# Kernel tuning notes

Hardware: AMD Instinct MI355X
Metric: run time of the kernel (lower is better)

Reference implementation:

```python
import jax, jax.numpy as jnp
import numpy as np
import math

ROPE_THETA = 10000.0


def apply_rope(x, positions):
    # x: [B, H, S, d_k], positions: [S]
    d_k = x.shape[-1]
    inv_freq = 1.0 / (ROPE_THETA ** (jnp.arange(0, d_k, 2, dtype=jnp.float32) / d_k))  # [d_k/2]
    angles = positions.astype(jnp.float32)[:, None] * inv_freq[None, :]  # [S, d_k/2]
    cos = jnp.cos(angles)
    sin = jnp.sin(angles)
    x1 = x[..., 0::2]
    x2 = x[..., 1::2]
    r1 = x1 * cos - x2 * sin
    r2 = x1 * sin + x2 * cos
    out = jnp.stack([r1, r2], axis=-1)  # interleave pairs back
    return out.reshape(x.shape)


def setup_inputs() -> dict:
    key = jax.random.key(0)
    k1, k2, k3 = jax.random.split(key, 3)
    B, S, D = 4, 2048, 1024
    x = jax.random.normal(k1, (B, S, D), dtype=jnp.float32)
    token_positions = jnp.arange(S, dtype=jnp.int32)
    w_qkv = jax.random.normal(k2, (3 * D, D), dtype=jnp.float32) * (1.0 / math.sqrt(D))
    w_o = jax.random.normal(k3, (D, D), dtype=jnp.float32) * (1.0 / math.sqrt(D))
    return {"x": x, "token_positions": token_positions, "w_qkv": w_qkv, "w_o": w_o}


def reference(x, token_positions, w_qkv, w_o):
    B, S, D = x.shape
    H = 16
    d_k = D // H
    qkv = jnp.einsum('bsd,ed->bse', x, w_qkv)  # [B, S, 3D]
    # rearrange '... s (stack h dk) -> stack ... h s dk'
    qkv = qkv.reshape(B, S, 3, H, d_k)
    q = jnp.transpose(qkv[:, :, 0], (0, 2, 1, 3))  # [B, H, S, dk]
    k = jnp.transpose(qkv[:, :, 1], (0, 2, 1, 3))
    v = jnp.transpose(qkv[:, :, 2], (0, 2, 1, 3))
    q = apply_rope(q, token_positions)
    k = apply_rope(k, token_positions)
    scores = jnp.einsum('bhqd,bhkd->bhqk', q, k) / math.sqrt(d_k)
    causal = jnp.tril(jnp.ones((S, S), dtype=bool))
    scores = jnp.where(causal[None, None], scores, -jnp.inf)
    attn = jax.nn.softmax(scores, axis=-1)
    out = jnp.einsum('bhqk,bhkd->bhqd', attn, v)  # [B, H, S, dk]
    out = jnp.transpose(out, (0, 2, 1, 3)).reshape(B, S, D)
    return jnp.einsum('bsd,ed->bse', out, w_o)
```

## Files before the change

kernel.cpp:

```cpp
#include <hip/hip_runtime.h>
#include <hip/hip_bf16.h>
#include <math.h>

typedef __bf16 bf16_t;
typedef __attribute__((ext_vector_type(8))) __bf16 bf16x8;
typedef __attribute__((ext_vector_type(4))) __bf16 bf16x4;
typedef __attribute__((ext_vector_type(4))) float f32x4;

#define MFMA_16x16x32(A_, B_, C_) __builtin_amdgcn_mfma_f32_16x16x32_bf16((A_), (B_), (C_), 0, 0, 0)

#define Bsz 4
#define Ssz 2048
#define Dsz 1024
#define Hh 16
#define DKd 64
#define Mrows (Bsz * Ssz)
#define N1 (3 * Dsz)
#define KD Dsz

static __device__ __forceinline__ float fast_exp2(float x) {
  float r;
  asm("v_exp_f32 %0, %1" : "=v"(r) : "v"(x));
  return r;
}

__global__ void prep_kernel(const float* __restrict__ x, const float* __restrict__ wqkv,
                            const float* __restrict__ wo, const int* __restrict__ pos,
                            bf16_t* __restrict__ xb, bf16_t* __restrict__ wqkvb,
                            bf16_t* __restrict__ wob, float2* __restrict__ tab) {
  constexpr int N4X = Mrows * KD / 4;
  constexpr int N4W = N1 * KD / 4;
  constexpr int N4O = Dsz * KD / 4;
  constexpr int NRT = Ssz * 32;
  const int i = blockIdx.x * blockDim.x + threadIdx.x;
  if (i < N4X) {
    float4 v = reinterpret_cast<const float4*>(x)[i];
    bf16x4 o = {(bf16_t)v.x, (bf16_t)v.y, (bf16_t)v.z, (bf16_t)v.w};
    reinterpret_cast<bf16x4*>(xb)[i] = o;
  } else if (i < N4X + N4W) {
    const int j = i - N4X;
    float4 v = reinterpret_cast<const float4*>(wqkv)[j];
    bf16x4 o = {(bf16_t)v.x, (bf16_t)v.y, (bf16_t)v.z, (bf16_t)v.w};
    reinterpret_cast<bf16x4*>(wqkvb)[j] = o;
  } else if (i < N4X + N4W + N4O) {
    const int j = i - N4X - N4W;
    float4 v = reinterpret_cast<const float4*>(wo)[j];
    bf16x4 o = {(bf16_t)v.x, (bf16_t)v.y, (bf16_t)v.z, (bf16_t)v.w};
    reinterpret_cast<bf16x4*>(wob)[j] = o;
  } else if (i < N4X + N4W + N4O + NRT) {
    const int j = i - N4X - N4W - N4O;
    const int s = j >> 5, f = j & 31;
    float inv_freq = powf(10000.0f, -(float)(2 * f) / 64.0f);
    float a = (float)pos[s] * inv_freq;
    tab[j] = make_float2(cosf(a), sinf(a));
  }
}

__global__ __launch_bounds__(512, 1) void gemm256_qkv_kernel(
    const bf16_t* __restrict__ A, const bf16_t* __restrict__ Bt,
    bf16_t* __restrict__ qb, bf16_t* __restrict__ kb, bf16_t* __restrict__ vtb,
    const float2* __restrict__ tab) {
  constexpr int NT = KD / 64;
  __shared__ __align__(16) bf16_t As[2][256 * 64];
  __shared__ __align__(16) bf16_t Bs[2][192 * 64];
  const int t = threadIdx.x;
  const int w = t >> 6, l = t & 63;
  const int lr = l & 15, lk = l >> 4;
  const int rs = lr >> 1;
  const int wm = w >> 2, wn = w & 3;
  const int m0 = blockIdx.y * 256, n0 = blockIdx.x * 192;

  const int gcol = ((t & 7) ^ ((t >> 4) & 7)) * 8;
  const bf16_t* gA = A + (size_t)(m0 + (t >> 3)) * KD + gcol;
  const bf16_t* gB = Bt + (size_t)(n0 + (t >> 3)) * KD + gcol;

  f32x4 acc[8][3] = {};
  bf16x8 bfv[3][2];

#define LDA_(I_, SB_, KT_)                                                        \
  __builtin_amdgcn_global_load_lds(gA + (size_t)(I_) * 64 * KD + (KT_),           \
                                   &As[SB_][((I_) * 64 + w * 8) * 64], 16, 0, 0)
#define LDB_(I_, SB_, KT_)                                                        \
  __builtin_amdgcn_global_load_lds(gB + (size_t)(I_) * 64 * KD + (KT_),           \
                                   &Bs[SB_][((I_) * 64 + w * 8) * 64], 16, 0, 0)

#define PH(BUF_, P_, STG0_, STG1_, VMW_)                                          \
  do {                                                                            \
    if ((P_) == 0) {                                                              \
      _Pragma("unroll") for (int n_ = 0; n_ < 3; ++n_) {                          \
        const int R_ = wn * 48 + n_ * 16 + lr;                                    \
        bfv[n_][0] = *reinterpret_cast<const bf16x8*>(                            \
            &Bs[BUF_][R_ * 64 + ((lk ^ rs) * 8)]);                                \
        bfv[n_][1] = *reinterpret_cast<const bf16x8*>(                            \
            &Bs[BUF_][R_ * 64 + (((4 + lk) ^ rs) * 8)]);                          \
      }                                                                           \
    }                                                                             \
    bf16x8 af0_[2], af1_[2];                                                      \
    {                                                                             \
      const int Ra_ = wm * 128 + (P_) * 32 + lr;                                  \
      const int Rb_ = Ra_ + 16;                                                   \
      af0_[0] = *reinterpret_cast<const bf16x8*>(&As[BUF_][Ra_ * 64 + ((lk ^ rs) * 8)]);       \
      af0_[1] = *reinterpret_cast<const bf16x8*>(&As[BUF_][Ra_ * 64 + (((4 + lk) ^ rs) * 8)]); \
      af1_[0] = *reinterpret_cast<const bf16x8*>(&As[BUF_][Rb_ * 64 + ((lk ^ rs) * 8)]);       \
      af1_[1] = *reinterpret_cast<const bf16x8*>(&As[BUF_][Rb_ * 64 + (((4 + lk) ^ rs) * 8)]); \
    }                                                                             \
    STG0_;                                                                        \
    STG1_;                                                                        \
    __builtin_amdgcn_s_barrier();                                                 \
    asm volatile("s_waitcnt lgkmcnt(0)" ::: "memory");                            \
    __builtin_amdgcn_sched_barrier(0);                                            \
    __builtin_amdgcn_s_setprio(1);                                                \
    _Pragma("unroll") for (int n_ = 0; n_ < 3; ++n_) {                            \
      acc[(P_)*2][n_] = MFMA_16x16x32(af0_[0], bfv[n_][0], acc[(P_)*2][n_]);      \
      acc[(P_)*2][n_] = MFMA_16x16x32(af0_[1], bfv[n_][1], acc[(P_)*2][n_]);      \
      acc[(P_)*2 + 1][n_] = MFMA_16x16x32(af1_[0], bfv[n_][0], acc[(P_)*2 + 1][n_]); \
      acc[(P_)*2 + 1][n_] = MFMA_16x16x32(af1_[1], bfv[n_][1], acc[(P_)*2 + 1][n_]); \
    }                                                                             \
    __builtin_amdgcn_s_setprio(0);                                                \
    VMW_;                                                                         \
    __builtin_amdgcn_s_barrier();                                                 \
  } while (0)

#define VM4_ do { asm volatile("s_waitcnt vmcnt(4)" ::: "memory"); __builtin_amdgcn_sched_barrier(0); } while (0)
#define VM2_ do { asm volatile("s_waitcnt vmcnt(2)" ::: "memory"); __builtin_amdgcn_sched_barrier(0); } while (0)

#define TILE_(BUF_, KTN_)                                                         \
  do {                                                                            \
    PH(BUF_, 0, LDB_(0, (BUF_) ^ 1, KTN_), LDB_(1, (BUF_) ^ 1, KTN_), (void)0);   \
    PH(BUF_, 1, LDB_(2, (BUF_) ^ 1, KTN_), LDA_(0, (BUF_) ^ 1, KTN_), VM4_);      \
    PH(BUF_, 2, LDA_(2, (BUF_) ^ 1, KTN_), LDA_(1, (BUF_) ^ 1, KTN_), (void)0);   \
    PH(BUF_, 3, LDA_(3, (BUF_) ^ 1, KTN_), (void)0, VM2_);                        \
  } while (0)

  LDB_(0, 0, 0); LDB_(1, 0, 0); LDB_(2, 0, 0);
  LDA_(0, 0, 0); LDA_(2, 0, 0); LDA_(1, 0, 0); LDA_(3, 0, 0);
  asm volatile("s_waitcnt vmcnt(2)" ::: "memory");
  __builtin_amdgcn_s_barrier();

#pragma unroll 1
  for (int tt = 0; tt < NT; tt += 2) {
    const int ktn0 = ((tt + 1) & (NT - 1)) * 64;
    TILE_(0, ktn0);
    const int ktn1 = ((tt + 2) & (NT - 1)) * 64;
    TILE_(1, ktn1);
  }
#undef TILE_
#undef VM4_
#undef VM2_
#undef PH
#undef LDA_
#undef LDB_

#pragma unroll
  for (int n = 0; n < 3; ++n) {
    const int colbase = n0 + wn * 48 + n * 16;
    const int sect = colbase >> 10;
    const int h = (colbase >> 6) & 15;
    const int dk = (colbase & 63) + lr;
    if (sect < 2) {
      bf16_t* dst0 = (sect == 0) ? qb : kb;
#pragma unroll
      for (int m = 0; m < 8; ++m)
#pragma unroll
        for (int r = 0; r < 4; ++r) {
          const int grow = m0 + wm * 128 + m * 16 + lk * 4 + r;
          const int bb = grow >> 11, s = grow & (Ssz - 1);
          const float v = acc[m][n][r];
          const float pv = __shfl_xor(v, 1);
          const float2 cs = tab[(s << 5) | (dk >> 1)];
          float vr = (dk & 1) ? (pv * cs.y + v * cs.x) : (v * cs.x - pv * cs.y);
          if (sect == 0) vr *= 0.18033688f;
          dst0[((size_t)(bb * Hh + h) * Ssz + s) * DKd + dk] = (bf16_t)vr;
        }
    } else {
#pragma unroll
      for (int m = 0; m < 8; ++m) {
        const int grow0 = m0 + wm * 128 + m * 16 + lk * 4;
        const int bb = grow0 >> 11, s0 = grow0 & (Ssz - 1);
        const bf16x4 ov = {(bf16_t)acc[m][n][0], (bf16_t)acc[m][n][1],
                           (bf16_t)acc[m][n][2], (bf16_t)acc[m][n][3]};
        *reinterpret_cast<bf16x4*>(
            vtb + ((size_t)(bb * Hh + h) * DKd + dk) * Ssz + s0) = ov;
      }
    }
  }
}

__global__ __launch_bounds__(512, 1) void gemm_out_kernel(
    const bf16_t* __restrict__ A, const bf16_t* __restrict__ Bt,
    float* __restrict__ fout) {
  constexpr int NT = KD / 64;
  __shared__ __align__(16) bf16_t As[2][256 * 64];
  __shared__ __align__(16) bf16_t Bs[2][128 * 64];
  const int t = threadIdx.x;
  const int w = t >> 6, l = t & 63;
  const int lr = l & 15, lk = l >> 4;
  const int rs = lr >> 1;
  const int wm = w >> 2, wn = w & 3;
  const int m0 = blockIdx.y * 256, n0 = blockIdx.x * 128;

  const int gcol = ((t & 7) ^ ((t >> 4) & 7)) * 8;
  const bf16_t* gA = A + (size_t)(m0 + (t >> 3)) * KD + gcol;
  const bf16_t* gB = Bt + (size_t)(n0 + (t >> 3)) * KD + gcol;

  f32x4 acc[8][2] = {};
  bf16x8 bfv[2][2];

#define OLDA_(I_, SB_, KT_)                                                       \
  __builtin_amdgcn_global_load_lds(gA + (size_t)(I_) * 64 * KD + (KT_),           \
                                   &As[SB_][((I_) * 64 + w * 8) * 64], 16, 0, 0)
#define OLDB_(I_, SB_, KT_)                                                       \
  __builtin_amdgcn_global_load_lds(gB + (size_t)(I_) * 64 * KD + (KT_),           \
                                   &Bs[SB_][((I_) * 64 + w * 8) * 64], 16, 0, 0)

#define OPH(BUF_, P_, STG0_, STG1_, VMW_)                                         \
  do {                                                                            \
    if ((P_) == 0) {                                                              \
      _Pragma("unroll") for (int n_ = 0; n_ < 2; ++n_) {                          \
        const int R_ = wn * 32 + n_ * 16 + lr;                                    \
        bfv[n_][0] = *reinterpret_cast<const bf16x8*>(                            \
            &Bs[BUF_][R_ * 64 + ((lk ^ rs) * 8)]);                                \
        bfv[n_][1] = *reinterpret_cast<const bf16x8*>(                            \
            &Bs[BUF_][R_ * 64 + (((4 + lk) ^ rs) * 8)]);                          \
      }                                                                           \
    }                                                                             \
    bf16x8 af0_[2], af1_[2];                                                      \
    {                                                                             \
      const int Ra_ = wm * 128 + (P_) * 32 + lr;                                  \
      const int Rb_ = Ra_ + 16;                                                   \
      af0_[0] = *reinterpret_cast<const bf16x8*>(&As[BUF_][Ra_ * 64 + ((lk ^ rs) * 8)]);       \
      af0_[1] = *reinterpret_cast<const bf16x8*>(&As[BUF_][Ra_ * 64 + (((4 + lk) ^ rs) * 8)]); \
      af1_[0] = *reinterpret_cast<const bf16x8*>(&As[BUF_][Rb_ * 64 + ((lk ^ rs) * 8)]);       \
      af1_[1] = *reinterpret_cast<const bf16x8*>(&As[BUF_][Rb_ * 64 + (((4 + lk) ^ rs) * 8)]); \
    }                                                                             \
    STG0_;                                                                        \
    STG1_;                                                                        \
    __builtin_amdgcn_s_barrier();                                                 \
    asm volatile("s_waitcnt lgkmcnt(0)" ::: "memory");                            \
    __builtin_amdgcn_sched_barrier(0);                                            \
    __builtin_amdgcn_s_setprio(1);                                                \
    _Pragma("unroll") for (int n_ = 0; n_ < 2; ++n_) {                            \
      acc[(P_)*2][n_] = MFMA_16x16x32(af0_[0], bfv[n_][0], acc[(P_)*2][n_]);      \
      acc[(P_)*2][n_] = MFMA_16x16x32(af0_[1], bfv[n_][1], acc[(P_)*2][n_]);      \
      acc[(P_)*2 + 1][n_] = MFMA_16x16x32(af1_[0], bfv[n_][0], acc[(P_)*2 + 1][n_]); \
      acc[(P_)*2 + 1][n_] = MFMA_16x16x32(af1_[1], bfv[n_][1], acc[(P_)*2 + 1][n_]); \
    }                                                                             \
    __builtin_amdgcn_s_setprio(0);                                                \
    VMW_;                                                                         \
    __builtin_amdgcn_s_barrier();                                                 \
  } while (0)

#define OVM4_ do { asm volatile("s_waitcnt vmcnt(4)" ::: "memory"); __builtin_amdgcn_sched_barrier(0); } while (0)
#define OVM2_ do { asm volatile("s_waitcnt vmcnt(2)" ::: "memory"); __builtin_amdgcn_sched_barrier(0); } while (0)

#define OTILE_(BUF_, KTN_)                                                        \
  do {                                                                            \
    OPH(BUF_, 0, OLDB_(0, (BUF_) ^ 1, KTN_), OLDB_(1, (BUF_) ^ 1, KTN_), (void)0);\
    OPH(BUF_, 1, OLDA_(0, (BUF_) ^ 1, KTN_), OLDA_(2, (BUF_) ^ 1, KTN_), OVM4_);  \
    OPH(BUF_, 2, OLDA_(1, (BUF_) ^ 1, KTN_), OLDA_(3, (BUF_) ^ 1, KTN_), (void)0);\
    OPH(BUF_, 3, (void)0, (void)0, OVM2_);                                        \
  } while (0)

  OLDB_(0, 0, 0); OLDB_(1, 0, 0);
  OLDA_(0, 0, 0); OLDA_(2, 0, 0); OLDA_(1, 0, 0); OLDA_(3, 0, 0);
  asm volatile("s_waitcnt vmcnt(2)" ::: "memory");
  __builtin_amdgcn_s_barrier();

#pragma unroll 1
  for (int tt = 0; tt < NT; tt += 2) {
    const int ktn0 = ((tt + 1) & (NT - 1)) * 64;
    OTILE_(0, ktn0);
    const int ktn1 = ((tt + 2) & (NT - 1)) * 64;
    OTILE_(1, ktn1);
  }
#undef OTILE_
#undef OVM4_
#undef OVM2_
#undef OPH
#undef OLDA_
#undef OLDB_

#pragma unroll
  for (int m = 0; m < 8; ++m)
#pragma unroll
    for (int r = 0; r < 4; ++r) {
      const int grow = m0 + wm * 128 + m * 16 + lk * 4 + r;
      float* op = fout + (size_t)grow * Dsz + n0 + wn * 32 + lr;
      op[0] = acc[m][0][r];
      op[16] = acc[m][1][r];
    }
}

__global__ __launch_bounds__(256, 3) void attn_kernel(
    const bf16_t* __restrict__ qb, const bf16_t* __restrict__ kb,
    const bf16_t* __restrict__ vtb, bf16_t* __restrict__ aout) {
  __shared__ __align__(16) bf16_t Ks[2][64 * 64];
  __shared__ __align__(16) bf16_t Vs[2][64 * 64];
  const int t = threadIdx.x, w = t >> 6, l = t & 63;
  const int lr = l & 15, lk = l >> 4;
  const int bid = blockIdx.x;
  const int bh = (bid & 7) * 8 + ((bid >> 3) & 7);
  const int qt = 15 - (bid >> 6);
  const int q0 = qt * 128;
  const int sub0 = q0 + w * 32;

  const bf16_t* qbase = qb + ((size_t)bh * Ssz + sub0) * DKd;
  bf16x8 qf[2][2];
#pragma unroll
  for (int s = 0; s < 2; ++s) {
    qf[s][0] = *reinterpret_cast<const bf16x8*>(qbase + (s * 16 + lr) * DKd + lk * 8);
    qf[s][1] = *reinterpret_cast<const bf16x8*>(qbase + (s * 16 + lr) * DKd + 32 + lk * 8);
  }

  f32x4 o[2][4] = {};
  float mrow[2] = {-INFINITY, -INFINITY};
  float lsum[2] = {0.f, 0.f};

  const int srow = t >> 2;
  const int scc = (t & 3) * 2;
  const bf16_t* kg = kb + ((size_t)bh * Ssz + srow) * DKd + scc * 8;
  const bf16_t* vg = vtb + ((size_t)bh * DKd + srow) * Ssz + scc * 8;
  const int koff0 = srow * 64 + ((scc ^ (srow & 7)) * 8);
  const int koff1 = srow * 64 + (((scc + 1) ^ (srow & 7)) * 8);
  int voff[4];
#pragma unroll
  for (int u = 0; u < 2; ++u) {
    const int c = scc + u;
    const int B = 32 * (c >> 2) + 16 * (c & 1) + 4 * ((c & 3) >> 1);
    const int ch = B >> 3, off = B & 7;
    voff[2 * u] = srow * 64 + ((ch ^ (srow & 7)) * 8) + off;
    voff[2 * u + 1] = srow * 64 + (((ch + 1) ^ (srow & 7)) * 8) + off;
  }

  const int fx0 = (lk ^ (lr & 7)) * 8;
  const int fx1 = ((lk + 4) ^ (lr & 7)) * 8;
  const int frow = lr * 64;

  const int kvend = q0 + 128;
  bf16x8 pk0 = *reinterpret_cast<const bf16x8*>(kg);
  bf16x8 pk1 = *reinterpret_cast<const bf16x8*>(kg + 8);
  bf16x8 pv0 = *reinterpret_cast<const bf16x8*>(vg);
  bf16x8 pv1 = *reinterpret_cast<const bf16x8*>(vg + 8);

  *reinterpret_cast<bf16x8*>(&Ks[0][koff0]) = pk0;
  *reinterpret_cast<bf16x8*>(&Ks[0][koff1]) = pk1;
  *reinterpret_cast<bf16x4*>(&Vs[0][voff[0]]) = __builtin_shufflevector(pv0, pv0, 0, 1, 2, 3);
  *reinterpret_cast<bf16x4*>(&Vs[0][voff[1]]) = __builtin_shufflevector(pv0, pv0, 4, 5, 6, 7);
  *reinterpret_cast<bf16x4*>(&Vs[0][voff[2]]) = __builtin_shufflevector(pv1, pv1, 0, 1, 2, 3);
  *reinterpret_cast<bf16x4*>(&Vs[0][voff[3]]) = __builtin_shufflevector(pv1, pv1, 4, 5, 6, 7);
  __syncthreads();

  for (int kv = 0; kv < kvend; kv += 64) {
    const int buf = (kv >> 6) & 1;
    const bool more = (kv + 64 < kvend);
    if (more) {
      pk0 = *reinterpret_cast<const bf16x8*>(kg + (size_t)(kv + 64) * DKd);
      pk1 = *reinterpret_cast<const bf16x8*>(kg + (size_t)(kv + 64) * DKd + 8);
      pv0 = *reinterpret_cast<const bf16x8*>(vg + kv + 64);
      pv1 = *reinterpret_cast<const bf16x8*>(vg + kv + 64 + 8);
    }
    const bf16_t* Kb = Ks[buf];
    const bf16_t* Vb = Vs[buf];
    bf16x8 kf0[4], kf1[4];
#pragma unroll
    for (int n = 0; n < 4; ++n) {
      kf0[n] = *reinterpret_cast<const bf16x8*>(Kb + frow + n * 1024 + fx0);
      kf1[n] = *reinterpret_cast<const bf16x8*>(Kb + frow + n * 1024 + fx1);
    }
    f32x4 sa[2][4];
#pragma unroll
    for (int s = 0; s < 2; ++s) {
      if (kv > sub0 + s * 16 + 15) continue;
#pragma unroll
      for (int n = 0; n < 4; ++n) {
        f32x4 z = {};
        z = MFMA_16x16x32(kf0[n], qf[s][0], z);
        z = MFMA_16x16x32(kf1[n], qf[s][1], z);
        sa[s][n] = z;
      }
    }
    bf16x8 pb[2][2];
#pragma unroll
    for (int s = 0; s < 2; ++s) {
      const int subrow = sub0 + s * 16;
      if (kv > subrow + 15) continue;
      if (kv + 63 > subrow) {
        const int qrow = subrow + lr;
        const int kbase = kv + lk * 4;
#pragma unroll
        for (int n = 0; n < 4; ++n)
#pragma unroll
          for (int r = 0; r < 4; ++r)
            if (kbase + n * 16 + r > qrow) sa[s][n][r] = -INFINITY;
      }
      float mx = fmaxf(fmaxf(fmaxf(sa[s][0][0], sa[s][0][1]), fmaxf(sa[s][0][2], sa[s][0][3])),
                       fmaxf(fmaxf(sa[s][1][0], sa[s][1][1]), fmaxf(sa[s][1][2], sa[s][1][3])));
      mx = fmaxf(mx, fmaxf(fmaxf(fmaxf(sa[s][2][0], sa[s][2][1]), fmaxf(sa[s][2][2], sa[s][2][3])),
                           fmaxf(fmaxf(sa[s][3][0], sa[s][3][1]), fmaxf(sa[s][3][2], sa[s][3][3]))));
      mx = fmaxf(mx, __shfl_xor(mx, 16));
      mx = fmaxf(mx, __shfl_xor(mx, 32));
      if (!__all(mx <= mrow[s] + 8.0f)) {
        const float mnew = fmaxf(mrow[s], mx);
        const float scl = fast_exp2(mrow[s] - mnew);
        mrow[s] = mnew;
        lsum[s] *= scl;
#pragma unroll
        for (int n = 0; n < 4; ++n)
#pragma unroll
          for (int r = 0; r < 4; ++r) o[s][n][r] *= scl;
      }
      float ps = 0.f;
#pragma unroll
      for (int n = 0; n < 4; ++n)
#pragma unroll
        for (int r = 0; r < 4; ++r) {
          const float p = fast_exp2(sa[s][n][r] - mrow[s]);
          sa[s][n][r] = p;
          ps += p;
        }
      lsum[s] += ps;
#pragma unroll
      for (int r = 0; r < 4; ++r) {
        pb[s][0][r] = (bf16_t)sa[s][0][r];
        pb[s][0][4 + r] = (bf16_t)sa[s][1][r];
        pb[s][1][r] = (bf16_t)sa[s][2][r];
        pb[s][1][4 + r] = (bf16_t)sa[s][3][r];
      }
    }
    bf16x8 vf0[4], vf1[4];
#pragma unroll
    for (int n = 0; n < 4; ++n) {
      vf0[n] = *reinterpret_cast<const bf16x8*>(Vb + frow + n * 1024 + fx0);
      vf1[n] = *reinterpret_cast<const bf16x8*>(Vb + frow + n * 1024 + fx1);
    }
#pragma unroll
    for (int s = 0; s < 2; ++s) {
      if (kv > sub0 + s * 16 + 15) continue;
#pragma unroll
      for (int n = 0; n < 4; ++n) {
        o[s][n] = MFMA_16x16x32(vf0[n], pb[s][0], o[s][n]);
        o[s][n] = MFMA_16x16x32(vf1[n], pb[s][1], o[s][n]);
      }
    }
    if (more) {
      bf16_t* Kn = Ks[buf ^ 1];
      bf16_t* Vn = Vs[buf ^ 1];
      *reinterpret_cast<bf16x8*>(&Kn[koff0]) = pk0;
      *reinterpret_cast<bf16x8*>(&Kn[koff1]) = pk1;
      *reinterpret_cast<bf16x4*>(&Vn[voff[0]]) = __builtin_shufflevector(pv0, pv0, 0, 1, 2, 3);
      *reinterpret_cast<bf16x4*>(&Vn[voff[1]]) = __builtin_shufflevector(pv0, pv0, 4, 5, 6, 7);
      *reinterpret_cast<bf16x4*>(&Vn[voff[2]]) = __builtin_shufflevector(pv1, pv1, 0, 1, 2, 3);
      *reinterpret_cast<bf16x4*>(&Vn[voff[3]]) = __builtin_shufflevector(pv1, pv1, 4, 5, 6, 7);
      __syncthreads();
    }
  }
  const int b_ = bh >> 4, h_ = bh & 15;
#pragma unroll
  for (int s = 0; s < 2; ++s) {
    float sm = lsum[s];
    sm += __shfl_xor(sm, 16);
    sm += __shfl_xor(sm, 32);
    const float inv = 1.0f / sm;
    const int qrow = sub0 + s * 16 + lr;
    bf16_t* op = aout + ((size_t)b_ * Ssz + qrow) * Dsz + h_ * DKd + lk * 4;
#pragma unroll
    for (int n = 0; n < 4; ++n) {
      const bf16x4 ov = {(bf16_t)(o[s][n][0] * inv), (bf16_t)(o[s][n][1] * inv),
                         (bf16_t)(o[s][n][2] * inv), (bf16_t)(o[s][n][3] * inv)};
      *reinterpret_cast<bf16x4*>(op + n * 16) = ov;
    }
  }
}

extern "C" void kernel_launch(void* const* d_in, const int* in_sizes, int n_in,
                              void* d_out, int out_size, void* d_ws, size_t ws_size,
                              hipStream_t stream) {
  const float* x = (const float*)d_in[0];
  const int* pos = (const int*)d_in[1];
  const float* wqkv = (const float*)d_in[2];
  const float* wo = (const float*)d_in[3];
  float* out = (float*)d_out;

  bf16_t* xb = (bf16_t*)d_ws;
  bf16_t* wqkvb = xb + (size_t)Mrows * KD;
  bf16_t* wob = wqkvb + (size_t)N1 * KD;
  bf16_t* qbuf = wob + (size_t)Dsz * KD;
  bf16_t* kbuf = qbuf + (size_t)64 * Ssz * DKd;
  bf16_t* vtb = kbuf + (size_t)64 * Ssz * DKd;
  float2* tab = (float2*)(vtb + (size_t)64 * Ssz * DKd);
  bf16_t* aout = xb;

  {
    constexpr int total = Mrows * KD / 4 + N1 * KD / 4 + Dsz * KD / 4 + Ssz * 32;
    prep_kernel<<<(total + 255) / 256, 256, 0, stream>>>(x, wqkv, wo, pos, xb, wqkvb, wob, tab);
  }

  gemm256_qkv_kernel<<<dim3(N1 / 192, Mrows / 256), 512, 0, stream>>>(
      xb, wqkvb, qbuf, kbuf, vtb, tab);

  attn_kernel<<<dim3(16 * 64), 256, 0, stream>>>(qbuf, kbuf, vtb, aout);

  gemm_out_kernel<<<dim3(Dsz / 128, Mrows / 256), 512, 0, stream>>>(
      aout, wob, out);
}
```

Before: 177.8 us.

## Process KV in 128-wide pairs per barrier and compute row sums via MFMA

Loads and double-buffers two 64-row K/V chunks per iteration, halving the number of __syncthreads and prefetch rounds. The softmax denominator is now accumulated by an MFMA against a ones vector on the bf16 probabilities, replacing scalar adds and cross-lane shuffles. Shared memory per block doubles and prefetch registers increase, which may reduce occupancy.

```diff
diff --git a/kernel.cpp b/kernel.cpp
--- a/kernel.cpp
+++ b/kernel.cpp
@@ -294,8 +294,8 @@
 __global__ __launch_bounds__(256, 3) void attn_kernel(
     const bf16_t* __restrict__ qb, const bf16_t* __restrict__ kb,
     const bf16_t* __restrict__ vtb, bf16_t* __restrict__ aout) {
-  __shared__ __align__(16) bf16_t Ks[2][64 * 64];
-  __shared__ __align__(16) bf16_t Vs[2][64 * 64];
+  __shared__ __align__(16) bf16_t Ks[2][2][64 * 64];
+  __shared__ __align__(16) bf16_t Vs[2][2][64 * 64];
   const int t = threadIdx.x, w = t >> 6, l = t & 63;
   const int lr = l & 15, lk = l >> 4;
   const int bid = blockIdx.x;
@@ -303,6 +303,7 @@
   const int qt = 15 - (bid >> 6);
   const int q0 = qt * 128;
   const int sub0 = q0 + w * 32;
+  const int npairs = qt + 1;
 
   const bf16_t* qbase = qb + ((size_t)bh * Ssz + sub0) * DKd;
   bf16x8 qf[2][2];
@@ -311,10 +312,13 @@
     qf[s][0] = *reinterpret_cast<const bf16x8*>(qbase + (s * 16 + lr) * DKd + lk * 8);
     qf[s][1] = *reinterpret_cast<const bf16x8*>(qbase + (s * 16 + lr) * DKd + 32 + lk * 8);
   }
+  bf16x8 ones;
+#pragma unroll
+  for (int i = 0; i < 8; ++i) ones[i] = (bf16_t)1.0f;
 
   f32x4 o[2][4] = {};
+  f32x4 lacc[2] = {};
   float mrow[2] = {-INFINITY, -INFINITY};
-  float lsum[2] = {0.f, 0.f};
 
   const int srow = t >> 2;
   const int scc = (t & 3) * 2;
@@ -336,131 +340,139 @@
   const int fx1 = ((lk + 4) ^ (lr & 7)) * 8;
   const int frow = lr * 64;
 
-  const int kvend = q0 + 128;
-  bf16x8 pk0 = *reinterpret_cast<const bf16x8*>(kg);
-  bf16x8 pk1 = *reinterpret_cast<const bf16x8*>(kg + 8);
-  bf16x8 pv0 = *reinterpret_cast<const bf16x8*>(vg);
-  bf16x8 pv1 = *reinterpret_cast<const bf16x8*>(vg + 8);
-
-  *reinterpret_cast<bf16x8*>(&Ks[0][koff0]) = pk0;
-  *reinterpret_cast<bf16x8*>(&Ks[0][koff1]) = pk1;
-  *reinterpret_cast<bf16x4*>(&Vs[0][voff[0]]) = __builtin_shufflevector(pv0, pv0, 0, 1, 2, 3);
-  *reinterpret_cast<bf16x4*>(&Vs[0][voff[1]]) = __builtin_shufflevector(pv0, pv0, 4, 5, 6, 7);
-  *reinterpret_cast<bf16x4*>(&Vs[0][voff[2]]) = __builtin_shufflevector(pv1, pv1, 0, 1, 2, 3);
-  *reinterpret_cast<bf16x4*>(&Vs[0][voff[3]]) = __builtin_shufflevector(pv1, pv1, 4, 5, 6, 7);
+  bf16x8 pk[2][2], pv[2][2];
+
+#define LOAD_PAIR_(P_)                                                            \
+  do {                                                                            \
+    _Pragma("unroll") for (int c_ = 0; c_ < 2; ++c_) {                            \
+      const size_t kvo_ = (size_t)((P_) * 128 + c_ * 64);                         \
+      pk[c_][0] = *reinterpret_cast<const bf16x8*>(kg + kvo_ * DKd);              \
+      pk[c_][1] = *reinterpret_cast<const bf16x8*>(kg + kvo_ * DKd + 8);          \
+      pv[c_][0] = *reinterpret_cast<const bf16x8*>(vg + kvo_);                    \
+      pv[c_][1] = *reinterpret_cast<const bf16x8*>(vg + kvo_ + 8);                \
+    }                                                                             \
+  } while (0)
+
+#define WRITE_PAIR_(SL_)                                                          \
+  do {                                                                            \
+    _Pragma("unroll") for (int c_ = 0; c_ < 2; ++c_) {                            \
+      *reinterpret_cast<bf16x8*>(&Ks[SL_][c_][koff0]) = pk[c_][0];                \
+      *reinterpret_cast<bf16x8*>(&Ks[SL_][c_][koff1]) = pk[c_][1];                \
+      *reinterpret_cast<bf16x4*>(&Vs[SL_][c_][voff[0]]) =                         \
+          __builtin_shufflevector(pv[c_][0], pv[c_][0], 0, 1, 2, 3);              \
+      *reinterpret_cast<bf16x4*>(&Vs[SL_][c_][voff[1]]) =                         \
+          __builtin_shufflevector(pv[c_][0], pv[c_][0], 4, 5, 6, 7);              \
+      *reinterpret_cast<bf16x4*>(&Vs[SL_][c_][voff[2]]) =                         \
+          __builtin_shufflevector(pv[c_][1], pv[c_][1], 0, 1, 2, 3);              \
+      *reinterpret_cast<bf16x4*>(&Vs[SL_][c_][voff[3]]) =                         \
+          __builtin_shufflevector(pv[c_][1], pv[c_][1], 4, 5, 6, 7);              \
+    }                                                                             \
+  } while (0)
+
+  LOAD_PAIR_(0);
+  WRITE_PAIR_(0);
   __syncthreads();
 
-  for (int kv = 0; kv < kvend; kv += 64) {
-    const int buf = (kv >> 6) & 1;
-    const bool more = (kv + 64 < kvend);
-    if (more) {
-      pk0 = *reinterpret_cast<const bf16x8*>(kg + (size_t)(kv + 64) * DKd);
-      pk1 = *reinterpret_cast<const bf16x8*>(kg + (size_t)(kv + 64) * DKd + 8);
-      pv0 = *reinterpret_cast<const bf16x8*>(vg + kv + 64);
-      pv1 = *reinterpret_cast<const bf16x8*>(vg + kv + 64 + 8);
-    }
-    const bf16_t* Kb = Ks[buf];
-    const bf16_t* Vb = Vs[buf];
-    bf16x8 kf0[4], kf1[4];
-#pragma unroll
-    for (int n = 0; n < 4; ++n) {
-      kf0[n] = *reinterpret_cast<const bf16x8*>(Kb + frow + n * 1024 + fx0);
-      kf1[n] = *reinterpret_cast<const bf16x8*>(Kb + frow + n * 1024 + fx1);
-    }
-    f32x4 sa[2][4];
-#pragma unroll
-    for (int s = 0; s < 2; ++s) {
-      if (kv > sub0 + s * 16 + 15) continue;
+  for (int p = 0; p < npairs; ++p) {
+    const int slot = p & 1;
+    const bool more = (p + 1 < npairs);
+    if (more) LOAD_PAIR_(p + 1);
+#pragma unroll
+    for (int c = 0; c < 2; ++c) {
+      const int kv = p * 128 + c * 64;
+      const bf16_t* Kb = Ks[slot][c];
+      const bf16_t* Vb = Vs[slot][c];
+      bf16x8 kf0[4], kf1[4];
 #pragma unroll
       for (int n = 0; n < 4; ++n) {
-        f32x4 z = {};
-        z = MFMA_16x16x32(kf0[n], qf[s][0], z);
-        z = MFMA_16x16x32(kf1[n], qf[s][1], z);
-        sa[s][n] = z;
+        kf0[n] = *reinterpret_cast<const bf16x8*>(Kb + frow + n * 1024 + fx0);
+        kf1[n] = *reinterpret_cast<const bf16x8*>(Kb + frow + n * 1024 + fx1);
       }
-    }
-    bf16x8 pb[2][2];
-#pragma unroll
-    for (int s = 0; s < 2; ++s) {
-      const int subrow = sub0 + s * 16;
-      if (kv > subrow + 15) continue;
-      if (kv + 63 > subrow) {
-        const int qrow = subrow + lr;
-        const int kbase = kv + lk * 4;
+      f32x4 sa[2][4];
+#pragma unroll
+      for (int s = 0; s < 2; ++s) {
+        if (kv > sub0 + s * 16 + 15) continue;
+#pragma unroll
+        for (int n = 0; n < 4; ++n) {
+          f32x4 z = {};
+          z = MFMA_16x16x32(kf0[n], qf[s][0], z);
+          z = MFMA_16x16x32(kf1[n], qf[s][1], z);
+          sa[s][n] = z;
+        }
+      }
+      bf16x8 pb[2][2];
+#pragma unroll
+      for (int s = 0; s < 2; ++s) {
+        const int subrow = sub0 + s * 16;
+        if (kv > subrow + 15) continue;
+        if (kv + 63 > subrow) {
+          const int qrow = subrow + lr;
+          const int kbase = kv + lk * 4;
+#pragma unroll
+          for (int n = 0; n < 4; ++n)
+#pragma unroll
+            for (int r = 0; r < 4; ++r)
+              if (kbase + n * 16 + r > qrow) sa[s][n][r] = -INFINITY;
+        }
+        float mx = fmaxf(fmaxf(fmaxf(sa[s][0][0], sa[s][0][1]), fmaxf(sa[s][0][2], sa[s][0][3])),
+                         fmaxf(fmaxf(sa[s][1][0], sa[s][1][1]), fmaxf(sa[s][1][2], sa[s][1][3])));
+        mx = fmaxf(mx, fmaxf(fmaxf(fmaxf(sa[s][2][0], sa[s][2][1]), fmaxf(sa[s][2][2], sa[s][2][3])),
+                             fmaxf(fmaxf(sa[s][3][0], sa[s][3][1]), fmaxf(sa[s][3][2], sa[s][3][3]))));
+        mx = fmaxf(mx, __shfl_xor(mx, 16));
+        mx = fmaxf(mx, __shfl_xor(mx, 32));
+        if (!__all(mx <= mrow[s] + 8.0f)) {
+          const float mnew = fmaxf(mrow[s], mx);
+          const float scl = fast_exp2(mrow[s] - mnew);
+          mrow[s] = mnew;
+#pragma unroll
+          for (int r = 0; r < 4; ++r) lacc[s][r] *= scl;
+#pragma unroll
+          for (int n = 0; n < 4; ++n)
+#pragma unroll
+            for (int r = 0; r < 4; ++r) o[s][n][r] *= scl;
+        }
 #pragma unroll
         for (int n = 0; n < 4; ++n)
 #pragma unroll
-          for (int r = 0; r < 4; ++r)
-            if (kbase + n * 16 + r > qrow) sa[s][n][r] = -INFINITY;
+          for (int r = 0; r < 4; ++r) sa[s][n][r] = fast_exp2(sa[s][n][r] - mrow[s]);
+#pragma unroll
+        for (int r = 0; r < 4; ++r) {
+          pb[s][0][r] = (bf16_t)sa[s][0][r];
+          pb[s][0][4 + r] = (bf16_t)sa[s][1][r];
+          pb[s][1][r] = (bf16_t)sa[s][2][r];
+          pb[s][1][4 + r] = (bf16_t)sa[s][3][r];
+        }
+        lacc[s] = MFMA_16x16x32(ones, pb[s][0], lacc[s]);
+        lacc[s] = MFMA_16x16x32(ones, pb[s][1], lacc[s]);
       }
-      float mx = fmaxf(fmaxf(fmaxf(sa[s][0][0], sa[s][0][1]), fmaxf(sa[s][0][2], sa[s][0][3])),
-                       fmaxf(fmaxf(sa[s][1][0], sa[s][1][1]), fmaxf(sa[s][1][2], sa[s][1][3])));
-      mx = fmaxf(mx, fmaxf(fmaxf(fmaxf(sa[s][2][0], sa[s][2][1]), fmaxf(sa[s][2][2], sa[s][2][3])),
-                           fmaxf(fmaxf(sa[s][3][0], sa[s][3][1]), fmaxf(sa[s][3][2], sa[s][3][3]))));
-      mx = fmaxf(mx, __shfl_xor(mx, 16));
-      mx = fmaxf(mx, __shfl_xor(mx, 32));
-      if (!__all(mx <= mrow[s] + 8.0f)) {
-        const float mnew = fmaxf(mrow[s], mx);
-        const float scl = fast_exp2(mrow[s] - mnew);
-        mrow[s] = mnew;
-        lsum[s] *= scl;
-#pragma unroll
-        for (int n = 0; n < 4; ++n)
-#pragma unroll
-          for (int r = 0; r < 4; ++r) o[s][n][r] *= scl;
+      bf16x8 vf0[4], vf1[4];
+#pragma unroll
+      for (int n = 0; n < 4; ++n) {
+        vf0[n] = *reinterpret_cast<const bf16x8*>(Vb + frow + n * 1024 + fx0);
+        vf1[n] = *reinterpret_cast<const bf16x8*>(Vb + frow + n * 1024 + fx1);
       }
-      float ps = 0.f;
-#pragma unroll
-      for (int n = 0; n < 4; ++n)
-#pragma unroll
-        for (int r = 0; r < 4; ++r) {
-          const float p = fast_exp2(sa[s][n][r] - mrow[s]);
-          sa[s][n][r] = p;
-          ps += p;
+#pragma unroll
+      for (int s = 0; s < 2; ++s) {
+        if (kv > sub0 + s * 16 + 15) continue;
+#pragma unroll
+        for (int n = 0; n < 4; ++n) {
+          o[s][n] = MFMA_16x16x32(vf0[n], pb[s][0], o[s][n]);
+          o[s][n] = MFMA_16x16x32(vf1[n], pb[s][1], o[s][n]);
         }
-      lsum[s] += ps;
-#pragma unroll
-      for (int r = 0; r < 4; ++r) {
-        pb[s][0][r] = (bf16_t)sa[s][0][r];
-        pb[s][0][4 + r] = (bf16_t)sa[s][1][r];
-        pb[s][1][r] = (bf16_t)sa[s][2][r];
-        pb[s][1][4 + r] = (bf16_t)sa[s][3][r];
-      }
-    }
-    bf16x8 vf0[4], vf1[4];
-#pragma unroll
-    for (int n = 0; n < 4; ++n) {
-      vf0[n] = *reinterpret_cast<const bf16x8*>(Vb + frow + n * 1024 + fx0);
-      vf1[n] = *reinterpret_cast<const bf16x8*>(Vb + frow + n * 1024 + fx1);
-    }
-#pragma unroll
-    for (int s = 0; s < 2; ++s) {
-      if (kv > sub0 + s * 16 + 15) continue;
-#pragma unroll
-      for (int n = 0; n < 4; ++n) {
-        o[s][n] = MFMA_16x16x32(vf0[n], pb[s][0], o[s][n]);
-        o[s][n] = MFMA_16x16x32(vf1[n], pb[s][1], o[s][n]);
       }
     }
     if (more) {
-      bf16_t* Kn = Ks[buf ^ 1];
-      bf16_t* Vn = Vs[buf ^ 1];
-      *reinterpret_cast<bf16x8*>(&Kn[koff0]) = pk0;
-      *reinterpret_cast<bf16x8*>(&Kn[koff1]) = pk1;
-      *reinterpret_cast<bf16x4*>(&Vn[voff[0]]) = __builtin_shufflevector(pv0, pv0, 0, 1, 2, 3);
-      *reinterpret_cast<bf16x4*>(&Vn[voff[1]]) = __builtin_shufflevector(pv0, pv0, 4, 5, 6, 7);
-      *reinterpret_cast<bf16x4*>(&Vn[voff[2]]) = __builtin_shufflevector(pv1, pv1, 0, 1, 2, 3);
-      *reinterpret_cast<bf16x4*>(&Vn[voff[3]]) = __builtin_shufflevector(pv1, pv1, 4, 5, 6, 7);
+      WRITE_PAIR_(slot ^ 1);
       __syncthreads();
     }
   }
+#undef LOAD_PAIR_
+#undef WRITE_PAIR_
+
   const int b_ = bh >> 4, h_ = bh & 15;
 #pragma unroll
   for (int s = 0; s < 2; ++s) {
-    float sm = lsum[s];
-    sm += __shfl_xor(sm, 16);
-    sm += __shfl_xor(sm, 32);
-    const float inv = 1.0f / sm;
+    const float inv = 1.0f / lacc[s][0];
     const int qrow = sub0 + s * 16 + lr;
     bf16_t* op = aout + ((size_t)b_ * Ssz + qrow) * Dsz + h_ * DKd + lk * 4;
 #pragma unroll
```

Measured after the change: 220.2 us. 1.24x slower.
